# Performance work log

Hardware: AMD Instinct MI355X
Metric: run time of the kernel (lower is better)

## Reference

```python
import jax, jax.numpy as jnp
import numpy as np

H = 16          # num_attention_heads
MEM = 1024      # memory bank tokens
NEG = jnp.float32(-1e30)


def setup_inputs() -> dict:
    key = jax.random.key(0)
    ks = jax.random.split(key, 4)
    B, T, C = 2, 2048, 2048
    x = jax.random.normal(ks[0], (B, T, C), dtype=jnp.float32)
    W_qkv = jax.random.normal(ks[1], (C, 3 * C), dtype=jnp.float32) * (1.0 / np.sqrt(C))
    b_qkv = jnp.zeros((3 * C,), dtype=jnp.float32)
    memory_bank = jax.random.normal(ks[2], (1, MEM, C), dtype=jnp.float32) * 0.02
    W_proj = jax.random.normal(ks[3], (C, C), dtype=jnp.float32) * (1.0 / np.sqrt(C))
    b_proj = jnp.zeros((C,), dtype=jnp.float32)
    return {"x": x, "W_qkv": W_qkv, "b_qkv": b_qkv, "memory_bank": memory_bank,
            "W_proj": W_proj, "b_proj": b_proj}


def reference(x, W_qkv, b_qkv, memory_bank, W_proj, b_proj):
    B, T, C = x.shape
    D = C // H
    M = memory_bank.shape[1]
    S = T + M
    # QKV projection and split
    qkv = x @ W_qkv + b_qkv                       # [B,T,3C]
    q, k, v = jnp.split(qkv, 3, axis=2)           # each [B,T,C]
    # Append (unprojected) memory bank tokens to K and V
    mem = jnp.broadcast_to(memory_bank, (B, M, C))
    k = jnp.concatenate([k, mem], axis=1)         # [B,S,C]
    v = jnp.concatenate([v, mem], axis=1)         # [B,S,C]
    # Split heads
    qh = q.reshape(B, T, H, D)
    kh = k.reshape(B, S, H, D)
    vh = v.reshape(B, S, H, D)
    # Scaled dot-product attention: causal over the T real tokens,
    # memory tokens (positions >= T) attendable by every query.
    scale = jnp.float32(1.0 / np.sqrt(D))
    scores = jnp.einsum('bthd,bshd->bhts', qh, kh) * scale   # [B,H,T,S]
    t_idx = jnp.arange(T)[:, None]
    s_idx = jnp.arange(S)[None, :]
    mask = (s_idx >= T) | (s_idx <= t_idx)        # [T,S]
    scores = jnp.where(mask[None, None], scores, NEG)
    attn = jax.nn.softmax(scores, axis=-1)
    out = jnp.einsum('bhts,bshd->bthd', attn, vh).reshape(B, T, C)
    return out @ W_proj + b_proj
```

## Files before the change

kernel.cpp:

```cpp
#include <hip/hip_runtime.h>
#include <math.h>

#define T_SEQ  2048
#define C_DIM  2048
#define H_NUM  16
#define D_HEAD 128
#define MEM_N  1024
#define S_ALL  3072
#define QKV_N  6144

typedef __attribute__((ext_vector_type(4))) float f32x4;
typedef __attribute__((ext_vector_type(8))) short bf16x8;
typedef __attribute__((ext_vector_type(8))) unsigned short us8;

__device__ __forceinline__ unsigned short f2bf(float f) {
    unsigned int u = __float_as_uint(f);
    u = (u + 0x7fffu + ((u >> 16) & 1u)) >> 16;
    return (unsigned short)u;
}

__device__ __forceinline__ void gload_lds16(const void* g, void* l) {
    __builtin_amdgcn_global_load_lds((const __attribute__((address_space(1))) void*)g,
                                     (__attribute__((address_space(3))) void*)l, 16, 0, 0);
}

__global__ __launch_bounds__(256, 2)
void split_w_t(const float* __restrict__ W, unsigned short* __restrict__ Th, int N)
{
    __shared__ float tile[64][68];
    const int tid = threadIdx.x;
    const int n0 = blockIdx.x << 6, k0 = blockIdx.y << 6;
    const int r = tid >> 2, c4 = (tid & 3) << 4;
    const float* src = W + (size_t)(k0 + r) * N + n0 + c4;
#pragma unroll
    for (int i = 0; i < 4; ++i)
        *(float4*)&tile[r][c4 + (i << 2)] = *(const float4*)(src + (i << 2));
    __syncthreads();
    unsigned int hi[8];
#pragma unroll
    for (int e = 0; e < 8; ++e) {
        const unsigned int h0 = f2bf(tile[c4 + 2 * e][r]);
        const unsigned int h1 = f2bf(tile[c4 + 2 * e + 1][r]);
        hi[e] = h0 | (h1 << 16);
    }
    unsigned short* dh = Th + (size_t)(n0 + r) * 2048 + k0 + c4;
    *(uint4*)dh       = make_uint4(hi[0], hi[1], hi[2], hi[3]);
    *(uint4*)(dh + 8) = make_uint4(hi[4], hi[5], hi[6], hi[7]);
}

__global__ __launch_bounds__(256, 2)
void split_mem_kernel(const float* __restrict__ mem, unsigned short* __restrict__ memb,
                      unsigned short* __restrict__ memt)
{
    __shared__ float tile[64][68];
    const int tid = threadIdx.x;
    const int c0 = blockIdx.x << 6, s0 = blockIdx.y << 6;
    const int r = tid >> 2, c4 = (tid & 3) << 4;
    const float* src = mem + (size_t)(s0 + r) * 2048 + c0 + c4;
    unsigned short* db = memb + (size_t)(s0 + r) * 2048 + c0 + c4;
#pragma unroll
    for (int i = 0; i < 4; ++i) {
        const float4 v = *(const float4*)(src + (i << 2));
        *(float4*)&tile[r][c4 + (i << 2)] = v;
        ushort4 o;
        o.x = f2bf(v.x); o.y = f2bf(v.y); o.z = f2bf(v.z); o.w = f2bf(v.w);
        *(ushort4*)(db + (i << 2)) = o;
    }
    __syncthreads();
    unsigned short* dt = memt + (size_t)(c0 + r) * 1024 + s0 + c4;
#pragma unroll
    for (int i = 0; i < 4; ++i) {
        ushort4 o;
        o.x = f2bf(tile[c4 + (i << 2) + 0][r]);
        o.y = f2bf(tile[c4 + (i << 2) + 1][r]);
        o.z = f2bf(tile[c4 + (i << 2) + 2][r]);
        o.w = f2bf(tile[c4 + (i << 2) + 3][r]);
        *(ushort4*)(dt + (i << 2)) = o;
    }
}

__global__ __launch_bounds__(256, 2)
void transpose_v_kernel(const unsigned short* __restrict__ Vr, unsigned short* __restrict__ Vrt)
{
    __shared__ unsigned short Vtmp[64 * 136];
    const int tid = threadIdx.x;
    const int s0 = (int)blockIdx.x << 6;
    const int h = blockIdx.y, b = blockIdx.z;
    const size_t bho = (size_t)(b * H_NUM + h) * (2048 * 128);
    const int sr = tid >> 2, ch = (tid & 3) << 5;
    const unsigned short* vp = Vr + bho + (size_t)(s0 + sr) * 128 + ch;
#pragma unroll
    for (int i = 0; i < 4; ++i)
        *(float4*)&Vtmp[sr * 136 + ch + (i << 3)] = *(const float4*)(vp + (i << 3));
    __syncthreads();
    const int d = tid >> 1, half = tid & 1;
    unsigned short* vd = Vrt + bho + (size_t)d * 2048 + s0 + (half << 5);
#pragma unroll
    for (int c = 0; c < 4; ++c) {
        us8 o;
#pragma unroll
        for (int j = 0; j < 8; ++j)
            o[j] = Vtmp[((half << 5) + (c << 3) + j) * 136 + d];
        *(us8*)(vd + (c << 3)) = o;
    }
}

__global__ __launch_bounds__(256, 3)
void gemm_qkv_mfma(const float* __restrict__ x,
                   const unsigned short* __restrict__ Bth,
                   const float* __restrict__ bias,
                   unsigned short* __restrict__ qb, unsigned short* __restrict__ Kr,
                   unsigned short* __restrict__ Vr)
{
    __shared__ unsigned short Ah[128 * 32], Al[128 * 32], Bh[128 * 32];
    const int tid = threadIdx.x;
    const int w = tid >> 6, lane = tid & 63, c16 = lane & 15, quad = lane >> 4;
    const int wm = w & 1, wn = w >> 1;
    const int bm = blockIdx.y << 7, bn = blockIdx.x << 7;

    const int ar = tid >> 1, ak = (tid & 1) << 4;
    const float* pA = x + (size_t)(bm + ar) * 2048 + ak;
    const int wofs = (tid >> 6) << 10;

    f32x4 acc[16];
#pragma unroll
    for (int i = 0; i < 16; ++i) acc[i] = (f32x4){0.f, 0.f, 0.f, 0.f};

    for (int kt = 0; kt < 2048; kt += 32) {
        float4 af[4];
#pragma unroll
        for (int i = 0; i < 4; ++i) af[i] = *(const float4*)(pA + kt + (i << 2));
        __syncthreads();
#pragma unroll
        for (int j = 0; j < 2; ++j) {
            const int c = (j << 8) + tid;
            const size_t go = (size_t)(bn + (c >> 2)) * 2048 + kt + ((c & 3) << 3);
            gload_lds16(Bth + go, (char*)Bh + (j << 12) + wofs);
        }
        const float* f = (const float*)af;
        unsigned int hp[8], lp[8];
#pragma unroll
        for (int e = 0; e < 8; ++e) {
            const unsigned int u0 = __float_as_uint(f[2 * e]), u1 = __float_as_uint(f[2 * e + 1]);
            const float l0 = f[2 * e]     - __uint_as_float(u0 & 0xFFFF0000u);
            const float l1 = f[2 * e + 1] - __uint_as_float(u1 & 0xFFFF0000u);
            hp[e] = (u0 >> 16) | (u1 & 0xFFFF0000u);
            lp[e] = (__float_as_uint(l0) >> 16) | (__float_as_uint(l1) & 0xFFFF0000u);
        }
        *(uint4*)&Ah[ar * 32 + ak]     = make_uint4(hp[0], hp[1], hp[2], hp[3]);
        *(uint4*)&Ah[ar * 32 + ak + 8] = make_uint4(hp[4], hp[5], hp[6], hp[7]);
        *(uint4*)&Al[ar * 32 + ak]     = make_uint4(lp[0], lp[1], lp[2], lp[3]);
        *(uint4*)&Al[ar * 32 + ak + 8] = make_uint4(lp[4], lp[5], lp[6], lp[7]);
        __syncthreads();

        bf16x8 a_h[4], a_l[4];
#pragma unroll
        for (int mt = 0; mt < 4; ++mt) {
            const int ao = (wm * 64 + mt * 16 + c16) * 32 + quad * 8;
            a_h[mt] = *(const bf16x8*)&Ah[ao];
            a_l[mt] = *(const bf16x8*)&Al[ao];
        }
#pragma unroll
        for (int nt = 0; nt < 4; ++nt) {
            const int bo = (wn * 64 + nt * 16 + c16) * 32 + quad * 8;
            const bf16x8 b_h = *(const bf16x8*)&Bh[bo];
#pragma unroll
            for (int mt = 0; mt < 4; ++mt) {
                acc[mt * 4 + nt] = __builtin_amdgcn_mfma_f32_16x16x32_bf16(a_h[mt], b_h, acc[mt * 4 + nt], 0, 0, 0);
                acc[mt * 4 + nt] = __builtin_amdgcn_mfma_f32_16x16x32_bf16(a_l[mt], b_h, acc[mt * 4 + nt], 0, 0, 0);
            }
        }
    }

    const int cls = bn >> 11;
    const float scl = (cls == 0) ? 0.08838834764831845f : 1.0f;
    const int h = (bn & 2047) >> 7;
    float bv[4];
#pragma unroll
    for (int nt = 0; nt < 4; ++nt) bv[nt] = bias[bn + wn * 64 + nt * 16 + c16];
#pragma unroll
    for (int mt = 0; mt < 4; ++mt) {
#pragma unroll
        for (int r = 0; r < 4; ++r) {
            const int rg = bm + wm * 64 + mt * 16 + quad * 4 + r;
            unsigned short* dst;
            if (cls == 0) {
                dst = qb + (size_t)rg * 2048 + bn;
            } else {
                const int bb = rg >> 11, t = rg & 2047;
                dst = (cls == 1 ? Kr : Vr) + (size_t)(bb * H_NUM + h) * (2048 * 128) + (size_t)t * 128;
            }
#pragma unroll
            for (int nt = 0; nt < 4; ++nt)
                dst[wn * 64 + nt * 16 + c16] = f2bf((acc[mt * 4 + nt][r] + bv[nt]) * scl);
        }
    }
}

__global__ __launch_bounds__(256, 3)
void gemm_proj_mfma(const unsigned short* __restrict__ Ahg, const unsigned short* __restrict__ Alg,
                    const unsigned short* __restrict__ Bth,
                    const float* __restrict__ bias, float* __restrict__ out)
{
    __shared__ unsigned short Ah[128 * 32], Al[128 * 32], Bh[128 * 32];
    const int tid = threadIdx.x;
    const int w = tid >> 6, lane = tid & 63, c16 = lane & 15, quad = lane >> 4;
    const int wm = w & 1, wn = w >> 1;
    const int bm = blockIdx.y << 7, bn = blockIdx.x << 7;
    const int wofs = (tid >> 6) << 10;

    f32x4 acc[16];
#pragma unroll
    for (int i = 0; i < 16; ++i) acc[i] = (f32x4){0.f, 0.f, 0.f, 0.f};

    for (int kt = 0; kt < 2048; kt += 32) {
        __syncthreads();
#pragma unroll
        for (int j = 0; j < 2; ++j) {
            const int c = (j << 8) + tid;
            const size_t ga = (size_t)(bm + (c >> 2)) * 2048 + kt + ((c & 3) << 3);
            const size_t gb = (size_t)(bn + (c >> 2)) * 2048 + kt + ((c & 3) << 3);
            gload_lds16(Ahg + ga, (char*)Ah + (j << 12) + wofs);
            gload_lds16(Alg + ga, (char*)Al + (j << 12) + wofs);
            gload_lds16(Bth + gb, (char*)Bh + (j << 12) + wofs);
        }
        __syncthreads();

        bf16x8 a_h[4], a_l[4];
#pragma unroll
        for (int mt = 0; mt < 4; ++mt) {
            const int ao = (wm * 64 + mt * 16 + c16) * 32 + quad * 8;
            a_h[mt] = *(const bf16x8*)&Ah[ao];
            a_l[mt] = *(const bf16x8*)&Al[ao];
        }
#pragma unroll
        for (int nt = 0; nt < 4; ++nt) {
            const int bo = (wn * 64 + nt * 16 + c16) * 32 + quad * 8;
            const bf16x8 b_h = *(const bf16x8*)&Bh[bo];
#pragma unroll
            for (int mt = 0; mt < 4; ++mt) {
                acc[mt * 4 + nt] = __builtin_amdgcn_mfma_f32_16x16x32_bf16(a_h[mt], b_h, acc[mt * 4 + nt], 0, 0, 0);
                acc[mt * 4 + nt] = __builtin_amdgcn_mfma_f32_16x16x32_bf16(a_l[mt], b_h, acc[mt * 4 + nt], 0, 0, 0);
            }
        }
    }

    float bv[4];
#pragma unroll
    for (int nt = 0; nt < 4; ++nt) bv[nt] = bias[bn + wn * 64 + nt * 16 + c16];
#pragma unroll
    for (int mt = 0; mt < 4; ++mt) {
#pragma unroll
        for (int r = 0; r < 4; ++r) {
            const int rg = bm + wm * 64 + mt * 16 + quad * 4 + r;
            float* dst = out + (size_t)rg * 2048 + bn + wn * 64 + c16;
#pragma unroll
            for (int nt = 0; nt < 4; ++nt)
                dst[nt * 16] = acc[mt * 4 + nt][r] + bv[nt];
        }
    }
}

__device__ __forceinline__ void stage_k(const unsigned short* __restrict__ kb, int kst,
                                        unsigned short* KsX, int w, int lane)
{
#pragma unroll
    for (int i = 0; i < 4; ++i) {
        const int o = (w << 12) + (i << 10) + (lane << 4);
        const int r = o >> 8;
        const int c = ((o >> 4) & 15) ^ (r & 7);
        gload_lds16(kb + (size_t)r * kst + (c << 3), (char*)KsX + (w << 12) + (i << 10));
    }
}
__device__ __forceinline__ void stage_v(const unsigned short* __restrict__ vb, int vst,
                                        unsigned short* VsX, int w, int lane)
{
#pragma unroll
    for (int i = 0; i < 4; ++i) {
        const int o = (w << 12) + (i << 10) + (lane << 4);
        const int r = o >> 7;
        const int c = ((o >> 4) & 7) ^ (r & 7);
        gload_lds16(vb + (size_t)r * vst + (c << 3), (char*)VsX + (w << 12) + (i << 10));
    }
}

__global__ __launch_bounds__(256, 2)
void attn_mfma_kernel(const unsigned short* __restrict__ qb,
                      const unsigned short* __restrict__ Kr,
                      const unsigned short* __restrict__ memb,
                      const unsigned short* __restrict__ Vrt,
                      const unsigned short* __restrict__ memt,
                      unsigned short* __restrict__ attn_h,
                      unsigned short* __restrict__ attn_l)
{
    __shared__ unsigned short lds[40960];
    unsigned short* Ks0 = lds;
    unsigned short* Ks1 = lds + 8192;
    unsigned short* Vs0 = lds + 16384;
    unsigned short* Vs1 = lds + 24576;
    unsigned short* Ps  = lds + 32768;
    unsigned short* Os  = lds;

    const int tid = threadIdx.x;
    const int w = tid >> 6, lane = tid & 63;
    const int c16 = lane & 15, quad = lane >> 4;
    const int bx = blockIdx.x;
    const int h = blockIdx.y, b = blockIdx.z;
    const int qt = b ? bx : (15 - bx);
    const int t0 = qt << 7;
    const int bT = b * T_SEQ;
    const int bh = b * H_NUM + h;

    const unsigned short* Krb = Kr + (size_t)bh * (2048 * 128);
    const unsigned short* Vrb = Vrt + (size_t)bh * (2048 * 128);
    const unsigned short* membh = memb + h * D_HEAD;
    const unsigned short* memth = memt + (size_t)h * D_HEAD * 1024;

    bf16x8 qfrag[2][4];
    {
        const int row = tid >> 1, co = (tid & 1) << 6;
        const unsigned short* src = qb + (size_t)(bT + t0 + row) * 2048 + h * D_HEAD + co;
#pragma unroll
        for (int i = 0; i < 8; ++i)
            *(float4*)&Os[row * 136 + co + (i << 3)] = *(const float4*)(src + (i << 3));
#pragma unroll
        for (int qi = 0; qi < 2; ++qi) {
            const int q = (w << 5) + qi * 16 + c16;
#pragma unroll
            for (int kk = 0; kk < 4; ++kk)
                qfrag[qi][kk] = *(const bf16x8*)&Os[q * 136 + (kk << 5) + (quad << 3)];
        }
    }
    __syncthreads();

    f32x4 acc_o[2][8];
#pragma unroll
    for (int qi = 0; qi < 2; ++qi)
#pragma unroll
        for (int i = 0; i < 8; ++i) acc_o[qi][i] = (f32x4){0.f, 0.f, 0.f, 0.f};
    float m_r[2] = {-1e30f, -1e30f};
    float l_r[2] = {0.f, 0.f};

    const int nk = (t0 >> 6) + 2;
    const int ntile = nk + (MEM_N >> 6);

    stage_k(Krb, 128, Ks0, w, lane);
    stage_v(Vrb, 2048, Vs0, w, lane);

    const int sw = c16 & 7;

    for (int it = 0; it < ntile; ++it) {
        __syncthreads();

        if (it + 1 < ntile) {
            const int nx = it + 1;
            const bool nm = nx >= nk;
            const int sl = (nm ? nx - nk : nx) << 6;
            const unsigned short* kb = nm ? membh + (size_t)sl * 2048 : Krb + (size_t)sl * 128;
            const unsigned short* vb = nm ? memth + sl : Vrb + sl;
            stage_k(kb, nm ? 2048 : 128, (it & 1) ? Ks0 : Ks1, w, lane);
            stage_v(vb, nm ? 1024 : 2048, (it & 1) ? Vs0 : Vs1, w, lane);
        }

        const unsigned short* Kc = (it & 1) ? Ks1 : Ks0;
        const unsigned short* Vc = (it & 1) ? Vs1 : Vs0;
        const bool mem_t = it >= nk;
        const int sl0 = (mem_t ? it - nk : it) << 6;
        const int s0 = mem_t ? T_SEQ + sl0 : sl0;

        const bool active = mem_t || (s0 <= t0 + (w << 5) + 31);
        if (active) {
            f32x4 acc_s[4][2];
#pragma unroll
            for (int nt = 0; nt < 4; ++nt)
#pragma unroll
                for (int qi = 0; qi < 2; ++qi) acc_s[nt][qi] = (f32x4){0.f, 0.f, 0.f, 0.f};

            bf16x8 ka[4][4];
#pragma unroll
            for (int nt = 0; nt < 4; ++nt) {
                const int rr = nt * 16 + c16;
#pragma unroll
                for (int kk = 0; kk < 4; ++kk)
                    ka[nt][kk] = *(const bf16x8*)&Kc[rr * 128 + ((((kk << 2) + quad) ^ sw) << 3)];
            }
            __builtin_amdgcn_s_setprio(1);
#pragma unroll
            for (int kk = 0; kk < 4; ++kk)
#pragma unroll
                for (int nt = 0; nt < 4; ++nt)
#pragma unroll
                    for (int qi = 0; qi < 2; ++qi)
                        acc_s[nt][qi] = __builtin_amdgcn_mfma_f32_16x16x32_bf16(ka[nt][kk], qfrag[qi][kk], acc_s[nt][qi], 0, 0, 0);
            __builtin_amdgcn_s_setprio(0);

            if (!mem_t && (s0 + 63 > t0 + (w << 5))) {
#pragma unroll
                for (int nt = 0; nt < 4; ++nt) {
                    const int sbase = s0 + nt * 16 + quad * 4;
#pragma unroll
                    for (int qi = 0; qi < 2; ++qi) {
                        const int q = t0 + (w << 5) + qi * 16 + c16;
#pragma unroll
                        for (int r = 0; r < 4; ++r)
                            if (sbase + r > q) acc_s[nt][qi][r] = -1e30f;
                    }
                }
            }

            float mx[2], al[2], rs[2];
#pragma unroll
            for (int qi = 0; qi < 2; ++qi) {
                float m0 = fmaxf(fmaxf(acc_s[0][qi][0], acc_s[0][qi][1]), fmaxf(acc_s[0][qi][2], acc_s[0][qi][3]));
#pragma unroll
                for (int nt = 1; nt < 4; ++nt)
                    m0 = fmaxf(m0, fmaxf(fmaxf(acc_s[nt][qi][0], acc_s[nt][qi][1]), fmaxf(acc_s[nt][qi][2], acc_s[nt][qi][3])));
                m0 = fmaxf(m0, __shfl_xor(m0, 16));
                m0 = fmaxf(m0, __shfl_xor(m0, 32));
                mx[qi] = m0;
            }
#pragma unroll
            for (int qi = 0; qi < 2; ++qi) {
                const float mn = fmaxf(m_r[qi], mx[qi]);
                al[qi] = __expf(m_r[qi] - mn);
                m_r[qi] = mn;
                float s = 0.f;
#pragma unroll
                for (int nt = 0; nt < 4; ++nt)
#pragma unroll
                    for (int r = 0; r < 4; ++r) {
                        const float p = __expf(acc_s[nt][qi][r] - mn);
                        acc_s[nt][qi][r] = p;
                        s += p;
                    }
                rs[qi] = s;
            }
#pragma unroll
            for (int qi = 0; qi < 2; ++qi) {
                rs[qi] += __shfl_xor(rs[qi], 16);
                rs[qi] += __shfl_xor(rs[qi], 32);
                l_r[qi] = l_r[qi] * al[qi] + rs[qi];
#pragma unroll
                for (int dt = 0; dt < 8; ++dt)
#pragma unroll
                    for (int r = 0; r < 4; ++r) acc_o[qi][dt][r] *= al[qi];
            }

#pragma unroll
            for (int qi = 0; qi < 2; ++qi) {
                const int q = (w << 5) + qi * 16 + c16;
                const int qx = (q & 7) << 4;
#pragma unroll
                for (int nt = 0; nt < 4; ++nt) {
                    ushort4 pk;
                    pk.x = f2bf(acc_s[nt][qi][0]); pk.y = f2bf(acc_s[nt][qi][1]);
                    pk.z = f2bf(acc_s[nt][qi][2]); pk.w = f2bf(acc_s[nt][qi][3]);
                    *(ushort4*)((char*)Ps + q * 128 + (((nt << 5) + (quad << 3)) ^ qx)) = pk;
                }
            }

            __builtin_amdgcn_s_setprio(1);
#pragma unroll
            for (int ks = 0; ks < 2; ++ks) {
                bf16x8 pb[2];
#pragma unroll
                for (int qi = 0; qi < 2; ++qi) {
                    const int q = (w << 5) + qi * 16 + c16;
                    pb[qi] = *(const bf16x8*)((char*)Ps + q * 128 + (((ks << 6) + (quad << 4)) ^ ((q & 7) << 4)));
                }
#pragma unroll
                for (int dt = 0; dt < 8; ++dt) {
                    const int rr = dt * 16 + c16;
                    const bf16x8 va = *(const bf16x8*)&Vc[rr * 64 + ((((ks << 2) + quad) ^ sw) << 3)];
                    acc_o[0][dt] = __builtin_amdgcn_mfma_f32_16x16x32_bf16(va, pb[0], acc_o[0][dt], 0, 0, 0);
                    acc_o[1][dt] = __builtin_amdgcn_mfma_f32_16x16x32_bf16(va, pb[1], acc_o[1][dt], 0, 0, 0);
                }
            }
            __builtin_amdgcn_s_setprio(0);
        }
    }

    __syncthreads();
    const float inv[2] = {1.0f / l_r[0], 1.0f / l_r[1]};
    const int row = tid >> 1, co = (tid & 1) << 6;
    unsigned short* gh = attn_h + (size_t)(bT + t0 + row) * 2048 + h * D_HEAD + co;
    unsigned short* gl = attn_l + (size_t)(bT + t0 + row) * 2048 + h * D_HEAD + co;

#pragma unroll
    for (int pass = 0; pass < 2; ++pass) {
#pragma unroll
        for (int qi = 0; qi < 2; ++qi) {
            const int q = (w << 5) + qi * 16 + c16;
#pragma unroll
            for (int dt = 0; dt < 8; ++dt) {
                ushort4 ov;
                unsigned short* po = (unsigned short*)&ov;
#pragma unroll
                for (int r = 0; r < 4; ++r) {
                    const float o = acc_o[qi][dt][r] * inv[qi];
                    const unsigned int u = __float_as_uint(o);
                    if (pass == 0) {
                        po[r] = (unsigned short)(u >> 16);
                    } else {
                        const float lo = o - __uint_as_float(u & 0xFFFF0000u);
                        po[r] = f2bf(lo);
                    }
                }
                *(ushort4*)&Os[q * 136 + dt * 16 + quad * 4] = ov;
            }
        }
        unsigned short* g = (pass == 0) ? gh : gl;
#pragma unroll
        for (int i = 0; i < 8; ++i)
            *(float4*)(g + (i << 3)) = *(const float4*)&Os[row * 136 + co + (i << 3)];
    }
}

extern "C" void kernel_launch(void* const* d_in, const int* in_sizes, int n_in,
                              void* d_out, int out_size, void* d_ws, size_t ws_size,
                              hipStream_t stream)
{
    const float* x     = (const float*)d_in[0];
    const float* Wqkv  = (const float*)d_in[1];
    const float* bqkv  = (const float*)d_in[2];
    const float* mem   = (const float*)d_in[3];
    const float* Wproj = (const float*)d_in[4];
    const float* bproj = (const float*)d_in[5];
    float* out = (float*)d_out;

    unsigned short* ws16 = (unsigned short*)d_ws;
    unsigned short* WqTh = ws16;
    unsigned short* rgn2 = WqTh + 12582912;
    unsigned short* qb   = rgn2 + 12582912;
    unsigned short* Kr   = qb   + 8388608;
    unsigned short* Vr   = Kr   + 8388608;
    unsigned short* Vrt  = Vr   + 8388608;
    unsigned short* memb = Vrt  + 8388608;
    unsigned short* memt = memb + 2097152;
    unsigned short* attn_h = WqTh;
    unsigned short* attn_l = rgn2;
    unsigned short* WpTh = rgn2 + 8388608;

    split_w_t<<<dim3(96, 32), 256, 0, stream>>>(Wqkv, WqTh, QKV_N);
    split_mem_kernel<<<dim3(32, 16), 256, 0, stream>>>(mem, memb, memt);

    gemm_qkv_mfma<<<dim3(48, 32), 256, 0, stream>>>(x, WqTh, bqkv, qb, Kr, Vr);

    split_w_t<<<dim3(32, 32), 256, 0, stream>>>(Wproj, WpTh, C_DIM);
    transpose_v_kernel<<<dim3(32, 16, 2), 256, 0, stream>>>(Vr, Vrt);

    attn_mfma_kernel<<<dim3(16, 16, 2), 256, 0, stream>>>(qb, Kr, memb, Vrt, memt, attn_h, attn_l);

    gemm_proj_mfma<<<dim3(16, 32), 256, 0, stream>>>(attn_h, attn_l, WpTh, bproj, out);
}
```

Measured before the change: 589.7 us.

## Pre-split x to bf16 hi/lo and double-buffer LDS in both GEMMs

Adds a kernel that splits x into bf16 high and low halves in global memory once, so the QKV GEMM can stream A through direct global-to-LDS loads instead of converting per tile. Both GEMMs now use two LDS buffers, prefetching the next K tile while MFMAs run on the current one, with one barrier per iteration. They also raise wave priority around the MFMA block. The cost is an extra pass over x plus more LDS per block (48KB), which may lower occupancy. Workspace regions are reused for the split x, so correctness depends on buffer lifetimes not overlapping.

Result: faster. 555.0 us (-5.9%).

```diff
diff --git a/kernel.cpp b/kernel.cpp
--- a/kernel.cpp
+++ b/kernel.cpp
@@ -24,6 +24,27 @@
                                      (__attribute__((address_space(3))) void*)l, 16, 0, 0);
 }
 
+__global__ __launch_bounds__(256, 4)
+void split_x_kernel(const float* __restrict__ x, unsigned short* __restrict__ Axh,
+                    unsigned short* __restrict__ Axl)
+{
+    const size_t base = ((size_t)blockIdx.x * 256 + threadIdx.x) * 8;
+    const float4 a = *(const float4*)(x + base);
+    const float4 b = *(const float4*)(x + base + 4);
+    float f[8] = {a.x, a.y, a.z, a.w, b.x, b.y, b.z, b.w};
+    unsigned int hp[4], lp[4];
+#pragma unroll
+    for (int e = 0; e < 4; ++e) {
+        const unsigned int u0 = __float_as_uint(f[2 * e]), u1 = __float_as_uint(f[2 * e + 1]);
+        const float l0 = f[2 * e]     - __uint_as_float(u0 & 0xFFFF0000u);
+        const float l1 = f[2 * e + 1] - __uint_as_float(u1 & 0xFFFF0000u);
+        hp[e] = (u0 >> 16) | (u1 & 0xFFFF0000u);
+        lp[e] = (__float_as_uint(l0) >> 16) | (__float_as_uint(l1) & 0xFFFF0000u);
+    }
+    *(uint4*)(Axh + base) = make_uint4(hp[0], hp[1], hp[2], hp[3]);
+    *(uint4*)(Axl + base) = make_uint4(lp[0], lp[1], lp[2], lp[3]);
+}
+
 __global__ __launch_bounds__(256, 2)
 void split_w_t(const float* __restrict__ W, unsigned short* __restrict__ Th, int N)
 {
@@ -106,53 +127,48 @@
 }
 
 __global__ __launch_bounds__(256, 3)
-void gemm_qkv_mfma(const float* __restrict__ x,
+void gemm_qkv_mfma(const unsigned short* __restrict__ Axh,
+                   const unsigned short* __restrict__ Axl,
                    const unsigned short* __restrict__ Bth,
                    const float* __restrict__ bias,
                    unsigned short* __restrict__ qb, unsigned short* __restrict__ Kr,
                    unsigned short* __restrict__ Vr)
 {
-    __shared__ unsigned short Ah[128 * 32], Al[128 * 32], Bh[128 * 32];
+    __shared__ unsigned short lds[6][4096];
     const int tid = threadIdx.x;
     const int w = tid >> 6, lane = tid & 63, c16 = lane & 15, quad = lane >> 4;
     const int wm = w & 1, wn = w >> 1;
     const int bm = blockIdx.y << 7, bn = blockIdx.x << 7;
-
-    const int ar = tid >> 1, ak = (tid & 1) << 4;
-    const float* pA = x + (size_t)(bm + ar) * 2048 + ak;
-    const int wofs = (tid >> 6) << 10;
+    const int wofs = w << 10;
 
     f32x4 acc[16];
 #pragma unroll
     for (int i = 0; i < 16; ++i) acc[i] = (f32x4){0.f, 0.f, 0.f, 0.f};
 
-    for (int kt = 0; kt < 2048; kt += 32) {
-        float4 af[4];
-#pragma unroll
-        for (int i = 0; i < 4; ++i) af[i] = *(const float4*)(pA + kt + (i << 2));
-        __syncthreads();
-#pragma unroll
-        for (int j = 0; j < 2; ++j) {
-            const int c = (j << 8) + tid;
-            const size_t go = (size_t)(bn + (c >> 2)) * 2048 + kt + ((c & 3) << 3);
-            gload_lds16(Bth + go, (char*)Bh + (j << 12) + wofs);
-        }
-        const float* f = (const float*)af;
-        unsigned int hp[8], lp[8];
-#pragma unroll
-        for (int e = 0; e < 8; ++e) {
-            const unsigned int u0 = __float_as_uint(f[2 * e]), u1 = __float_as_uint(f[2 * e + 1]);
-            const float l0 = f[2 * e]     - __uint_as_float(u0 & 0xFFFF0000u);
-            const float l1 = f[2 * e + 1] - __uint_as_float(u1 & 0xFFFF0000u);
-            hp[e] = (u0 >> 16) | (u1 & 0xFFFF0000u);
-            lp[e] = (__float_as_uint(l0) >> 16) | (__float_as_uint(l1) & 0xFFFF0000u);
-        }
-        *(uint4*)&Ah[ar * 32 + ak]     = make_uint4(hp[0], hp[1], hp[2], hp[3]);
-        *(uint4*)&Ah[ar * 32 + ak + 8] = make_uint4(hp[4], hp[5], hp[6], hp[7]);
-        *(uint4*)&Al[ar * 32 + ak]     = make_uint4(lp[0], lp[1], lp[2], lp[3]);
-        *(uint4*)&Al[ar * 32 + ak + 8] = make_uint4(lp[4], lp[5], lp[6], lp[7]);
-        __syncthreads();
-
+#define STAGE_QKV(buf, kt)                                                        \
+    do {                                                                          \
+        _Pragma("unroll") for (int j = 0; j < 2; ++j) {                           \
+            const int o = (j << 8) + tid;                                         \
+            const int r = o >> 2, cc = (o & 3) << 3;                              \
+            gload_lds16(Axh + (size_t)(bm + r) * 2048 + (kt) + cc,                \
+                        (char*)&lds[(buf) * 3 + 0][0] + (j << 12) + wofs);        \
+            gload_lds16(Axl + (size_t)(bm + r) * 2048 + (kt) + cc,                \
+                        (char*)&lds[(buf) * 3 + 1][0] + (j << 12) + wofs);        \
+            gload_lds16(Bth + (size_t)(bn + r) * 2048 + (kt) + cc,                \
+                        (char*)&lds[(buf) * 3 + 2][0] + (j << 12) + wofs);        \
+        }                                                                         \
+    } while (0)
+
+    STAGE_QKV(0, 0);
+    __syncthreads();
+
+    for (int t = 0; t < 64; ++t) {
+        const int cur = t & 1;
+        if (t + 1 < 64) STAGE_QKV(cur ^ 1, (t + 1) << 5);
+
+        const unsigned short* Ah = lds[cur * 3 + 0];
+        const unsigned short* Al = lds[cur * 3 + 1];
+        const unsigned short* Bh = lds[cur * 3 + 2];
         bf16x8 a_h[4], a_l[4];
 #pragma unroll
         for (int mt = 0; mt < 4; ++mt) {
@@ -160,6 +176,7 @@
             a_h[mt] = *(const bf16x8*)&Ah[ao];
             a_l[mt] = *(const bf16x8*)&Al[ao];
         }
+        __builtin_amdgcn_s_setprio(1);
 #pragma unroll
         for (int nt = 0; nt < 4; ++nt) {
             const int bo = (wn * 64 + nt * 16 + c16) * 32 + quad * 8;
@@ -170,6 +187,8 @@
                 acc[mt * 4 + nt] = __builtin_amdgcn_mfma_f32_16x16x32_bf16(a_l[mt], b_h, acc[mt * 4 + nt], 0, 0, 0);
             }
         }
+        __builtin_amdgcn_s_setprio(0);
+        __syncthreads();
     }
 
     const int cls = bn >> 11;
@@ -202,30 +221,41 @@
                     const unsigned short* __restrict__ Bth,
                     const float* __restrict__ bias, float* __restrict__ out)
 {
-    __shared__ unsigned short Ah[128 * 32], Al[128 * 32], Bh[128 * 32];
+    __shared__ unsigned short lds[6][4096];
     const int tid = threadIdx.x;
     const int w = tid >> 6, lane = tid & 63, c16 = lane & 15, quad = lane >> 4;
     const int wm = w & 1, wn = w >> 1;
     const int bm = blockIdx.y << 7, bn = blockIdx.x << 7;
-    const int wofs = (tid >> 6) << 10;
+    const int wofs = w << 10;
 
     f32x4 acc[16];
 #pragma unroll
     for (int i = 0; i < 16; ++i) acc[i] = (f32x4){0.f, 0.f, 0.f, 0.f};
 
-    for (int kt = 0; kt < 2048; kt += 32) {
-        __syncthreads();
-#pragma unroll
-        for (int j = 0; j < 2; ++j) {
-            const int c = (j << 8) + tid;
-            const size_t ga = (size_t)(bm + (c >> 2)) * 2048 + kt + ((c & 3) << 3);
-            const size_t gb = (size_t)(bn + (c >> 2)) * 2048 + kt + ((c & 3) << 3);
-            gload_lds16(Ahg + ga, (char*)Ah + (j << 12) + wofs);
-            gload_lds16(Alg + ga, (char*)Al + (j << 12) + wofs);
-            gload_lds16(Bth + gb, (char*)Bh + (j << 12) + wofs);
-        }
-        __syncthreads();
-
+#define STAGE_PROJ(buf, kt)                                                       \
+    do {                                                                          \
+        _Pragma("unroll") for (int j = 0; j < 2; ++j) {                           \
+            const int o = (j << 8) + tid;                                         \
+            const int r = o >> 2, cc = (o & 3) << 3;                              \
+            gload_lds16(Ahg + (size_t)(bm + r) * 2048 + (kt) + cc,                \
+                        (char*)&lds[(buf) * 3 + 0][0] + (j << 12) + wofs);        \
+            gload_lds16(Alg + (size_t)(bm + r) * 2048 + (kt) + cc,                \
+                        (char*)&lds[(buf) * 3 + 1][0] + (j << 12) + wofs);        \
+            gload_lds16(Bth + (size_t)(bn + r) * 2048 + (kt) + cc,                \
+                        (char*)&lds[(buf) * 3 + 2][0] + (j << 12) + wofs);        \
+        }                                                                         \
+    } while (0)
+
+    STAGE_PROJ(0, 0);
+    __syncthreads();
+
+    for (int t = 0; t < 64; ++t) {
+        const int cur = t & 1;
+        if (t + 1 < 64) STAGE_PROJ(cur ^ 1, (t + 1) << 5);
+
+        const unsigned short* Ah = lds[cur * 3 + 0];
+        const unsigned short* Al = lds[cur * 3 + 1];
+        const unsigned short* Bh = lds[cur * 3 + 2];
         bf16x8 a_h[4], a_l[4];
 #pragma unroll
         for (int mt = 0; mt < 4; ++mt) {
@@ -233,6 +263,7 @@
             a_h[mt] = *(const bf16x8*)&Ah[ao];
             a_l[mt] = *(const bf16x8*)&Al[ao];
         }
+        __builtin_amdgcn_s_setprio(1);
 #pragma unroll
         for (int nt = 0; nt < 4; ++nt) {
             const int bo = (wn * 64 + nt * 16 + c16) * 32 + quad * 8;
@@ -243,6 +274,8 @@
                 acc[mt * 4 + nt] = __builtin_amdgcn_mfma_f32_16x16x32_bf16(a_l[mt], b_h, acc[mt * 4 + nt], 0, 0, 0);
             }
         }
+        __builtin_amdgcn_s_setprio(0);
+        __syncthreads();
     }
 
     float bv[4];
@@ -540,11 +573,14 @@
     unsigned short* attn_h = WqTh;
     unsigned short* attn_l = rgn2;
     unsigned short* WpTh = rgn2 + 8388608;
-
+    unsigned short* Axh = rgn2;
+    unsigned short* Axl = Vrt;
+
+    split_x_kernel<<<dim3(4096), 256, 0, stream>>>(x, Axh, Axl);
     split_w_t<<<dim3(96, 32), 256, 0, stream>>>(Wqkv, WqTh, QKV_N);
     split_mem_kernel<<<dim3(32, 16), 256, 0, stream>>>(mem, memb, memt);
 
-    gemm_qkv_mfma<<<dim3(48, 32), 256, 0, stream>>>(x, WqTh, bqkv, qb, Kr, Vr);
+    gemm_qkv_mfma<<<dim3(48, 32), 256, 0, stream>>>(Axh, Axl, WqTh, bqkv, qb, Kr, Vr);
 
     split_w_t<<<dim3(32, 32), 256, 0, stream>>>(Wproj, WpTh, C_DIM);
     transpose_v_kernel<<<dim3(32, 16, 2), 256, 0, stream>>>(Vr, Vrt);
```
